# Performance work log

Hardware: AMD Instinct MI355X
Metric: run time of the kernel (lower is better)

The kernel has to match this reference:

```python
import jax, jax.numpy as jnp
import numpy as np

B, S, D = 2, 2048, 1024
H, HK, HD = 16, 4, 64          # query heads, kv heads, head dim = D//H
WIN = 1024                     # sliding attention window
E, K, DH = 8, 2, 2048          # experts, top_k, expert hidden (== d_head ctor arg)
ATTN_EPS, FFN_EPS = 1e-5, 1e-6
ROPE_THETA = 10000.0


def setup_inputs() -> dict:
    key = jax.random.key(0)
    ks = jax.random.split(key, 9)
    sc = 0.02
    # real rotary frequencies for positions [start_pos, start_pos+S)
    start_pos = 0
    inv_freq = 1.0 / (ROPE_THETA ** (jnp.arange(0, HD, 2, dtype=jnp.float32) / HD))  # [HD//2]
    pos = jnp.arange(start_pos, start_pos + S, dtype=jnp.float32)
    ang = pos[:, None] * inv_freq[None, :]  # [S, HD//2]
    return {
        'x': jax.random.normal(ks[0], (B, S, D), jnp.float32),
        'freqs_cos': jnp.cos(ang),
        'freqs_sin': jnp.sin(ang),
        'attn_norm_w': jnp.ones((D,), jnp.float32),
        'wq': jax.random.normal(ks[1], (D, H * HD), jnp.float32) * sc,
        'wk': jax.random.normal(ks[2], (D, HK * HD), jnp.float32) * sc,
        'wv': jax.random.normal(ks[3], (D, HK * HD), jnp.float32) * sc,
        'wo': jax.random.normal(ks[4], (H * HD, D), jnp.float32) * sc,
        'ffn_norm_w': jnp.ones((D,), jnp.float32),
        'router_w': jax.random.normal(ks[5], (D, E), jnp.float32) * sc,
        'w1': jax.random.normal(ks[6], (E, D, DH), jnp.float32) * sc,
        'w2': jax.random.normal(ks[7], (E, DH, D), jnp.float32) * sc,
        'start_pos': start_pos,
    }


def _rmsnorm(x, w, eps):
    return x * jax.lax.rsqrt(jnp.mean(x * x, axis=-1, keepdims=True) + eps) * w


def _rope(t, cos, sin):
    # t: [B,S,N,HD]; cos/sin: [S,HD//2] -> complex rotation on consecutive pairs
    shp = t.shape
    t = t.reshape(shp[:-1] + (HD // 2, 2))
    t0, t1 = t[..., 0], t[..., 1]
    c = cos[None, :, None, :]
    s = sin[None, :, None, :]
    r = jnp.stack([t0 * c - t1 * s, t0 * s + t1 * c], axis=-1)
    return r.reshape(shp)


def reference(x, freqs_cos, freqs_sin, attn_norm_w, wq, wk, wv, wo,
              ffn_norm_w, router_w, w1, w2, start_pos):
    # ---- attention sublayer (RMSNorm -> GQA sliding-window attn) ----
    hn = _rmsnorm(x, attn_norm_w, ATTN_EPS)
    q = (hn @ wq).reshape(B, S, H, HD)
    k = (hn @ wk).reshape(B, S, HK, HD)
    v = (hn @ wv).reshape(B, S, HK, HD)
    q = _rope(q, freqs_cos, freqs_sin)
    k = _rope(k, freqs_cos, freqs_sin)
    rep = H // HK
    k = jnp.repeat(k, rep, axis=2)  # [B,S,H,HD]
    v = jnp.repeat(v, rep, axis=2)
    scale = 1.0 / np.sqrt(HD).astype(np.float32)
    scores = jnp.einsum('bqhd,bkhd->bhqk', q, k) * scale  # [B,H,S,S]
    qi = jnp.arange(S) + start_pos
    kj = jnp.arange(S) + start_pos
    mask = (kj[None, :] <= qi[:, None]) & (qi[:, None] - kj[None, :] < WIN)
    scores = jnp.where(mask[None, None], scores, jnp.float32(-1e30))
    attn = jax.nn.softmax(scores, axis=-1)
    o = jnp.einsum('bhqk,bkhd->bqhd', attn, v).reshape(B, S, H * HD)
    h = x + o @ wo

    # ---- MoE sublayer (RMSNorm -> router top-k -> expert FFNs) ----
    fn = _rmsnorm(h, ffn_norm_w, FFN_EPS).reshape(-1, D)  # [T,D], T=B*S
    probs = jax.nn.softmax(fn @ router_w, axis=-1)        # [T,E]
    top_vals, top_idx = jax.lax.top_k(probs, K)           # [T,K]
    gates = top_vals / jnp.sum(top_vals, axis=-1, keepdims=True)
    gmat = jnp.sum(jax.nn.one_hot(top_idx, E, dtype=fn.dtype) * gates[..., None], axis=1)  # [T,E]
    moe = jnp.zeros_like(fn)
    for e in range(E):  # fixed small expert count
        moe = moe + gmat[:, e:e + 1] * (jax.nn.silu(fn @ w1[e]) @ w2[e])
    return h + moe.reshape(B, S, D)
```

## Files before the change

kernel.cpp:

```cpp
#include <hip/hip_runtime.h>
#include <hip/hip_bf16.h>

using bf16 = __hip_bfloat16;
typedef __attribute__((ext_vector_type(8))) short bf16x8;
typedef __attribute__((ext_vector_type(4))) short short4v;
typedef __attribute__((ext_vector_type(4))) float f32x4;

#define DEV static __device__ __forceinline__

DEV float b2f(bf16 v) { return __bfloat162float(v); }
DEV bf16  f2b(float f) { return __float2bfloat16(f); }
DEV short bbits(float f) { bf16 h = __float2bfloat16(f); short u; __builtin_memcpy(&u, &h, 2); return u; }
DEV float sb2f(short s) {
  unsigned u = ((unsigned)(unsigned short)s) << 16;
  float f; __builtin_memcpy(&f, &u, 4); return f;
}

#define GL2LDS(g, l)                                                        \
  __builtin_amdgcn_global_load_lds(                                         \
      (const __attribute__((address_space(1))) void*)(g),                   \
      (__attribute__((address_space(3))) void*)(l), 16, 0, 0)

__global__ __launch_bounds__(256) void transpose_convert(
    const float* __restrict__ src, bf16* __restrict__ dst, int K, int N) {
  __shared__ float tile[64][65];
  int n0 = blockIdx.x * 64, k0 = blockIdx.y * 64;
  size_t bo = (size_t)blockIdx.z * K * N;
  src += bo; dst += bo;
  int t = threadIdx.x;
  int rr = t >> 4, cc = (t & 15) * 4;
#pragma unroll
  for (int p = 0; p < 4; ++p) {
    int r = rr + p * 16;
    const float4 v = *(const float4*)&src[(size_t)(k0 + r) * N + n0 + cc];
    tile[r][cc] = v.x; tile[r][cc + 1] = v.y; tile[r][cc + 2] = v.z; tile[r][cc + 3] = v.w;
  }
  __syncthreads();
#pragma unroll
  for (int p = 0; p < 4; ++p) {
    int nr = rr + p * 16;
    short4v o;
    o[0] = bbits(tile[cc + 0][nr]);
    o[1] = bbits(tile[cc + 1][nr]);
    o[2] = bbits(tile[cc + 2][nr]);
    o[3] = bbits(tile[cc + 3][nr]);
    *(short4v*)&dst[(size_t)(n0 + nr) * K + k0 + cc] = o;
  }
}

__global__ __launch_bounds__(256) void rmsnorm_kernel(
    const float* __restrict__ x, const float* __restrict__ w,
    bf16* __restrict__ o, float eps) {
  int row = blockIdx.x;
  const float* xr = x + (size_t)row * 1024;
  int t = threadIdx.x;
  float4 v = *(const float4*)&xr[t * 4];
  float ss = v.x * v.x + v.y * v.y + v.z * v.z + v.w * v.w;
#pragma unroll
  for (int d = 32; d; d >>= 1) ss += __shfl_down(ss, d);
  __shared__ float red[4];
  if ((t & 63) == 0) red[t >> 6] = ss;
  __syncthreads();
  float sum = red[0] + red[1] + red[2] + red[3];
  float sc = rsqrtf(sum * (1.f / 1024.f) + eps);
  const float4 wv = *(const float4*)&w[t * 4];
  short4v pk;
  pk[0] = bbits(v.x * sc * wv.x);
  pk[1] = bbits(v.y * sc * wv.y);
  pk[2] = bbits(v.z * sc * wv.z);
  pk[3] = bbits(v.w * sc * wv.w);
  *(short4v*)&o[(size_t)row * 1024 + t * 4] = pk;
}

__global__ __launch_bounds__(256) void rope_kernel(
    bf16* __restrict__ tbuf, const float* __restrict__ fcos,
    const float* __restrict__ fsin, int ncols, int pshift) {
  int tid = blockIdx.x * 256 + threadIdx.x;
  int row = tid >> pshift;
  int cp = tid & ((1 << pshift) - 1);
  if (row >= 4096) return;
  int i = cp & 31;
  int s = row & 2047;
  bf16* p = tbuf + (size_t)row * ncols + cp * 2;
  float t0 = b2f(p[0]), t1 = b2f(p[1]);
  float c = fcos[s * 32 + i], sn = fsin[s * 32 + i];
  p[0] = f2b(t0 * c - t1 * sn);
  p[1] = f2b(t0 * sn + t1 * c);
}

template <int MODE>
__global__ __launch_bounds__(256) void gemm_bt(
    const bf16* __restrict__ A, const bf16* __restrict__ Bt,
    int M, int N, int Kd,
    bf16* __restrict__ outb, float* __restrict__ outf,
    const float* __restrict__ resid,
    const int* __restrict__ counts, const int* __restrict__ offsets,
    const int* __restrict__ tok, const float* __restrict__ gatel) {
  int count = M, off = 0;
  const bf16* Ap = A;
  const bf16* Bp = Bt;
  if (MODE == 2 || MODE == 3) {
    int e = blockIdx.z;
    count = counts[e]; off = offsets[e];
    Bp = Bt + (size_t)e * Kd * N;
    if (MODE == 3) Ap = A + (size_t)off * Kd;
  }
  int mb, nb;
  if (MODE == 2 || MODE == 3) {
    mb = blockIdx.y * 128; nb = blockIdx.x * 128;
  } else {
    int gx = gridDim.x;
    int flat = blockIdx.y * gx + blockIdx.x;
    int cpx = (gx * gridDim.y) >> 3;
    int swz = (flat & 7) * cpx + (flat >> 3);
    mb = (swz / gx) * 128; nb = (swz % gx) * 128;
  }
  if (mb >= count) return;

  __shared__ __align__(16) bf16 As[2][128 * 32];
  __shared__ __align__(16) bf16 Bs[2][128 * 32];

  int t = threadIdx.x;
  int lane = t & 63, wid = t >> 6;

  const bf16* agl[2];
  const bf16* bgl[2];
#pragma unroll
  for (int iss = 0; iss < 2; ++iss) {
    int p = iss * 256 + wid * 64 + lane;
    int row = p >> 2, cs = p & 3;
    int c = cs ^ (row & 3);
    int m = mb + row;
    const bf16* abase;
    if (MODE == 2) {
      int tokid = (m < count) ? tok[off + m] : 0;
      abase = A + (size_t)tokid * Kd;
    } else {
      int mm = (m < count) ? m : 0;
      abase = Ap + (size_t)mm * Kd;
    }
    agl[iss] = abase + c * 8;
    bgl[iss] = Bp + (size_t)(nb + row) * Kd + c * 8;
  }

  int wr = (wid >> 1) * 64, wc = (wid & 1) * 64;
  int lr = lane & 15, lkc = lane >> 4;

  auto stage = [&](int buf, int kt) {
#pragma unroll
    for (int iss = 0; iss < 2; ++iss) {
      GL2LDS(agl[iss] + kt * 32, &As[buf][(iss * 256 + wid * 64) * 8]);
      GL2LDS(bgl[iss] + kt * 32, &Bs[buf][(iss * 256 + wid * 64) * 8]);
    }
  };

  const f32x4 fzero = {0.f, 0.f, 0.f, 0.f};
  f32x4 acc[4][4];
#pragma unroll
  for (int i = 0; i < 4; ++i)
#pragma unroll
    for (int j = 0; j < 4; ++j) acc[i][j] = fzero;

  int nk = Kd >> 5;
  stage(0, 0);
  __syncthreads();
  for (int kt = 0; kt < nk; ++kt) {
    int cur = kt & 1;
    if (kt + 1 < nk) stage(cur ^ 1, kt + 1);
    bf16x8 af[4], bfr[4];
#pragma unroll
    for (int i = 0; i < 4; ++i) {
      int r = wr + i * 16 + lr;
      af[i] = *(const bf16x8*)&As[cur][r * 32 + ((lkc ^ (r & 3)) * 8)];
    }
#pragma unroll
    for (int j = 0; j < 4; ++j) {
      int r = wc + j * 16 + lr;
      bfr[j] = *(const bf16x8*)&Bs[cur][r * 32 + ((lkc ^ (r & 3)) * 8)];
    }
#pragma unroll
    for (int i = 0; i < 4; ++i)
#pragma unroll
      for (int j = 0; j < 4; ++j)
        acc[i][j] = __builtin_amdgcn_mfma_f32_16x16x32_bf16(af[i], bfr[j], acc[i][j], 0, 0, 0);
    __syncthreads();
  }

  int rq = lane >> 4;
#pragma unroll
  for (int i = 0; i < 4; ++i) {
#pragma unroll
    for (int j = 0; j < 4; ++j) {
      if (MODE == 4) {
        int n = nb + wc + j * 16 + lr;
        int kh = n >> 6, d = n & 63;
        int m0 = mb + wr + i * 16 + rq * 4;
        int bb = m0 >> 11, s = m0 & 2047;
        short4v pk;
#pragma unroll
        for (int r = 0; r < 4; ++r) pk[r] = bbits(acc[i][j][r]);
        *(short4v*)&outb[((size_t)((bb * 4 + kh) * 64 + d)) * 2048 + s] = pk;
      } else {
#pragma unroll
        for (int r = 0; r < 4; ++r) {
          int m = mb + wr + i * 16 + rq * 4 + r;
          int n = nb + wc + j * 16 + lr;
          float v = acc[i][j][r];
          if (MODE == 0) {
            outb[(size_t)m * N + n] = f2b(v);
          } else if (MODE == 1) {
            outf[(size_t)m * N + n] = resid[(size_t)m * N + n] + v;
          } else if (MODE == 2) {
            if (m < count) {
              float sg = 1.f / (1.f + expf(-v));
              outb[(size_t)(off + m) * N + n] = f2b(v * sg);
            }
          } else if (MODE == 3) {
            if (m < count) {
              int row = off + m;
              outb[(size_t)row * N + n] = f2b(gatel[row] * v);
            }
          }
        }
      }
    }
  }
}

__global__ __launch_bounds__(256) void attn_kernel(
    const bf16* __restrict__ q, const bf16* __restrict__ kb,
    const bf16* __restrict__ vt, bf16* __restrict__ o) {
  int qb = blockIdx.x, h = blockIdx.y, b = blockIdx.z;
  int kh = h >> 2;
  int t = threadIdx.x;
  int lane = t & 63, wid = t >> 6;
  int lr = lane & 15, lkc = lane >> 4;
  int q0 = qb * 64;
  int qrow = q0 + wid * 16;

  __shared__ __align__(16) bf16 Ks[64 * 64];
  __shared__ __align__(16) bf16 Vs[64 * 64];
  __shared__ __align__(16) bf16 Ps[4][16 * 72];

  bf16x8 aq[2];
#pragma unroll
  for (int kk = 0; kk < 2; ++kk)
    aq[kk] = *(const bf16x8*)&q[(size_t)(b * 2048 + qrow + lr) * 1024 + h * 64 + kk * 32 + lkc * 8];

  const f32x4 fzero = {0.f, 0.f, 0.f, 0.f};
  f32x4 oacc[4];
  float mrun[4], lrun[4];
#pragma unroll
  for (int r = 0; r < 4; ++r) { oacc[r] = fzero; mrun[r] = -1e30f; lrun[r] = 0.f; }

  int klo = q0 - 1023; if (klo < 0) klo = 0;
  int tlo = klo >> 6, thi = q0 >> 6;
  int skey = t >> 3;
  int sch = t & 7;

  for (int kt = tlo; kt <= thi; ++kt) {
    int kbase = kt * 64;
#pragma unroll
    for (int pp = 0; pp < 2; ++pp) {
      int key = skey + pp * 32;
      bf16x8 kv = *(const bf16x8*)&kb[(size_t)(b * 2048 + kbase + key) * 256 + kh * 64 + sch * 8];
      *(bf16x8*)&Ks[key * 64 + ((sch ^ (key & 7)) * 8)] = kv;
      bf16x8 vv = *(const bf16x8*)&vt[((size_t)((b * 4 + kh) * 64 + key)) * 2048 + kbase + sch * 8];
      *(bf16x8*)&Vs[key * 64 + ((sch ^ (key & 7)) * 8)] = vv;
    }
    __syncthreads();

    f32x4 sacc[4];
#pragma unroll
    for (int nt = 0; nt < 4; ++nt) sacc[nt] = fzero;
#pragma unroll
    for (int nt = 0; nt < 4; ++nt)
#pragma unroll
      for (int kk = 0; kk < 2; ++kk) {
        int r = nt * 16 + lr;
        bf16x8 bk = *(const bf16x8*)&Ks[r * 64 + (((kk * 4 + lkc) ^ (r & 7)) * 8)];
        sacc[nt] = __builtin_amdgcn_mfma_f32_16x16x32_bf16(aq[kk], bk, sacc[nt], 0, 0, 0);
      }

    float sval[4][4], mt[4];
    int qg = qrow + lkc * 4;
#pragma unroll
    for (int r = 0; r < 4; ++r) mt[r] = -1e30f;
#pragma unroll
    for (int nt = 0; nt < 4; ++nt) {
      int kkey = kbase + nt * 16 + lr;
#pragma unroll
      for (int r = 0; r < 4; ++r) {
        float s = sacc[nt][r] * 0.125f;
        int qq = qg + r;
        bool valid = (kkey <= qq) && (qq - kkey < 1024);
        s = valid ? s : -1e30f;
        sval[nt][r] = s;
        mt[r] = fmaxf(mt[r], s);
      }
    }
#pragma unroll
    for (int d = 1; d < 16; d <<= 1)
#pragma unroll
      for (int r = 0; r < 4; ++r) mt[r] = fmaxf(mt[r], __shfl_xor(mt[r], d));
    float alpha[4], rs[4];
#pragma unroll
    for (int r = 0; r < 4; ++r) {
      float mn = fmaxf(mrun[r], mt[r]);
      alpha[r] = __expf(mrun[r] - mn);
      mrun[r] = mn;
      rs[r] = 0.f;
    }
#pragma unroll
    for (int nt = 0; nt < 4; ++nt)
#pragma unroll
      for (int r = 0; r < 4; ++r) {
        float pv = __expf(sval[nt][r] - mrun[r]);
        sval[nt][r] = pv;
        rs[r] += pv;
      }
#pragma unroll
    for (int d = 1; d < 16; d <<= 1)
#pragma unroll
      for (int r = 0; r < 4; ++r) rs[r] += __shfl_xor(rs[r], d);
#pragma unroll
    for (int r = 0; r < 4; ++r) lrun[r] = lrun[r] * alpha[r] + rs[r];
#pragma unroll
    for (int dt = 0; dt < 4; ++dt) {
      f32x4 t4 = oacc[dt];
#pragma unroll
      for (int r = 0; r < 4; ++r) t4[r] *= alpha[r];
      oacc[dt] = t4;
    }

    bf16* pw = &Ps[wid][0];
#pragma unroll
    for (int nt = 0; nt < 4; ++nt)
#pragma unroll
      for (int r = 0; r < 4; ++r)
        pw[(lkc * 4 + r) * 72 + nt * 16 + lr] = f2b(sval[nt][r]);
    __syncthreads();

    bf16x8 pa[2];
#pragma unroll
    for (int kk2 = 0; kk2 < 2; ++kk2)
      pa[kk2] = *(const bf16x8*)&pw[lr * 72 + kk2 * 32 + lkc * 8];
#pragma unroll
    for (int dt = 0; dt < 4; ++dt)
#pragma unroll
      for (int kk2 = 0; kk2 < 2; ++kk2) {
        int rrow = dt * 16 + lr;
        bf16x8 bv = *(const bf16x8*)&Vs[rrow * 64 + (((kk2 * 4 + lkc) ^ (rrow & 7)) * 8)];
        oacc[dt] = __builtin_amdgcn_mfma_f32_16x16x32_bf16(pa[kk2], bv, oacc[dt], 0, 0, 0);
      }
    __syncthreads();
  }

#pragma unroll
  for (int dt = 0; dt < 4; ++dt)
#pragma unroll
    for (int r = 0; r < 4; ++r) {
      int qq = qrow + lkc * 4 + r;
      int dd = dt * 16 + lr;
      o[(size_t)(b * 2048 + qq) * 1024 + h * 64 + dd] = f2b(oacc[dt][r] / lrun[r]);
    }
}

__global__ __launch_bounds__(256) void router_kernel(
    const float* __restrict__ h, const float* __restrict__ ffnw,
    const float* __restrict__ rw, float* __restrict__ gates,
    int* __restrict__ eidx) {
  int wid = threadIdx.x >> 6, lane = threadIdx.x & 63;
  int row = blockIdx.x * 4 + wid;
  const float* hr = h + (size_t)row * 1024;
  float xs[16];
  float ss = 0.f;
#pragma unroll
  for (int i = 0; i < 16; ++i) { float f = hr[lane + i * 64]; xs[i] = f; ss += f * f; }
#pragma unroll
  for (int d = 32; d; d >>= 1) ss += __shfl_xor(ss, d);
  float sc = rsqrtf(ss * (1.f / 1024.f) + 1e-6f);
  float lg[8];
#pragma unroll
  for (int e = 0; e < 8; ++e) lg[e] = 0.f;
#pragma unroll
  for (int i = 0; i < 16; ++i) {
    int d = lane + i * 64;
    float f = xs[i] * sc * ffnw[d];
    const float* rr = rw + d * 8;
#pragma unroll
    for (int e = 0; e < 8; ++e) lg[e] += f * rr[e];
  }
#pragma unroll
  for (int d = 32; d; d >>= 1)
#pragma unroll
    for (int e = 0; e < 8; ++e) lg[e] += __shfl_xor(lg[e], d);
  if (lane == 0) {
    int e0 = 0; float v0 = lg[0];
#pragma unroll
    for (int e = 1; e < 8; ++e) if (lg[e] > v0) { v0 = lg[e]; e0 = e; }
    int e1 = -1; float v1 = -1e30f;
#pragma unroll
    for (int e = 0; e < 8; ++e) if (e != e0 && lg[e] > v1) { v1 = lg[e]; e1 = e; }
    float r1 = expf(v1 - v0);
    float den = 1.f + r1;
    gates[row * 2] = 1.f / den;
    gates[row * 2 + 1] = r1 / den;
    eidx[row * 2] = e0;
    eidx[row * 2 + 1] = e1;
  }
}

__global__ __launch_bounds__(1024) void moe_setup(
    const int* __restrict__ eidx, const float* __restrict__ gates,
    int* __restrict__ counts, int* __restrict__ offsets,
    int* __restrict__ tok, float* __restrict__ gatel, int* __restrict__ inv) {
  __shared__ int hist[8];
  __shared__ int cur[8];
  int t = threadIdx.x;
  if (t < 8) hist[t] = 0;
  __syncthreads();
  int e[8];
#pragma unroll
  for (int c = 0; c < 8; ++c) {
    e[c] = eidx[c * 1024 + t];
    atomicAdd(&hist[e[c]], 1);
  }
  __syncthreads();
  if (t == 0) {
    int o = 0;
#pragma unroll
    for (int i = 0; i < 8; ++i) {
      offsets[i] = o; cur[i] = o;
      int cnt = hist[i]; counts[i] = cnt; o += cnt;
    }
  }
  __syncthreads();
#pragma unroll
  for (int c = 0; c < 8; ++c) {
    int i = c * 1024 + t;
    int pos = atomicAdd(&cur[e[c]], 1);
    tok[pos] = i >> 1;
    gatel[pos] = gates[i];
    inv[i] = pos;
  }
}

__global__ __launch_bounds__(256) void final_add(
    const float* __restrict__ h, const bf16* __restrict__ y2,
    const int* __restrict__ inv, float* __restrict__ out) {
  int tokid = blockIdx.x;
  int t = threadIdx.x;
  int i0 = inv[tokid * 2], i1 = inv[tokid * 2 + 1];
  size_t base = (size_t)tokid * 1024 + t * 4;
  float4 a = *(const float4*)&h[base];
  short4v p0 = *(const short4v*)&y2[(size_t)i0 * 1024 + t * 4];
  short4v p1 = *(const short4v*)&y2[(size_t)i1 * 1024 + t * 4];
  float4 o;
  o.x = a.x + sb2f(p0[0]) + sb2f(p1[0]);
  o.y = a.y + sb2f(p0[1]) + sb2f(p1[1]);
  o.z = a.z + sb2f(p0[2]) + sb2f(p1[2]);
  o.w = a.w + sb2f(p0[3]) + sb2f(p1[3]);
  *(float4*)&out[base] = o;
}

extern "C" void kernel_launch(void* const* d_in, const int* in_sizes, int n_in,
                              void* d_out, int out_size, void* d_ws, size_t ws_size,
                              hipStream_t stream) {
  const float* x    = (const float*)d_in[0];
  const float* fcos = (const float*)d_in[1];
  const float* fsin = (const float*)d_in[2];
  const float* attw = (const float*)d_in[3];
  const float* wq   = (const float*)d_in[4];
  const float* wk   = (const float*)d_in[5];
  const float* wv   = (const float*)d_in[6];
  const float* wo   = (const float*)d_in[7];
  const float* ffnw = (const float*)d_in[8];
  const float* rw   = (const float*)d_in[9];
  const float* w1   = (const float*)d_in[10];
  const float* w2   = (const float*)d_in[11];
  float* out = (float*)d_out;

  const int M = 4096;
  char* p = (char*)d_ws;
  auto alloc = [&](size_t b) { char* r = p; p += (b + 255) & ~(size_t)255; return r; };

  bf16* hn    = (bf16*)alloc((size_t)M * 1024 * 2);
  bf16* qb    = (bf16*)alloc((size_t)M * 1024 * 2);
  bf16* kbuf  = (bf16*)alloc((size_t)M * 256 * 2);
  bf16* vt    = (bf16*)alloc((size_t)M * 256 * 2);
  bf16* ob    = (bf16*)alloc((size_t)M * 1024 * 2);
  float* hbuf = (float*)alloc((size_t)M * 1024 * 4);
  bf16* fn    = (bf16*)alloc((size_t)M * 1024 * 2);
  bf16* wqt   = (bf16*)alloc((size_t)1024 * 1024 * 2);
  bf16* wkt   = (bf16*)alloc((size_t)256 * 1024 * 2);
  bf16* wvt   = (bf16*)alloc((size_t)256 * 1024 * 2);
  bf16* wot   = (bf16*)alloc((size_t)1024 * 1024 * 2);
  bf16* w1t   = (bf16*)alloc((size_t)8 * 2048 * 1024 * 2);
  bf16* w2t   = (bf16*)alloc((size_t)8 * 1024 * 2048 * 2);
  bf16* act   = (bf16*)alloc((size_t)8192 * 2048 * 2);
  bf16* y2    = (bf16*)alloc((size_t)8192 * 1024 * 2);
  float* gates = (float*)alloc((size_t)M * 2 * 4);
  int* eidx    = (int*)alloc((size_t)M * 2 * 4);
  int* counts  = (int*)alloc(8 * 4);
  int* offsets = (int*)alloc(8 * 4);
  int* tok     = (int*)alloc(8192 * 4);
  int* inv     = (int*)alloc(8192 * 4);
  float* gatel = (float*)alloc(8192 * 4);

  transpose_convert<<<dim3(16, 16, 1), 256, 0, stream>>>(wq, wqt, 1024, 1024);
  transpose_convert<<<dim3(4, 16, 1), 256, 0, stream>>>(wk, wkt, 1024, 256);
  transpose_convert<<<dim3(4, 16, 1), 256, 0, stream>>>(wv, wvt, 1024, 256);
  transpose_convert<<<dim3(16, 16, 1), 256, 0, stream>>>(wo, wot, 1024, 1024);
  transpose_convert<<<dim3(32, 16, 8), 256, 0, stream>>>(w1, w1t, 1024, 2048);
  transpose_convert<<<dim3(16, 32, 8), 256, 0, stream>>>(w2, w2t, 2048, 1024);

  rmsnorm_kernel<<<M, 256, 0, stream>>>(x, attw, hn, 1e-5f);

  gemm_bt<0><<<dim3(8, 32, 1), 256, 0, stream>>>(hn, wqt, M, 1024, 1024, qb, nullptr, nullptr,
      nullptr, nullptr, nullptr, nullptr);
  gemm_bt<0><<<dim3(2, 32, 1), 256, 0, stream>>>(hn, wkt, M, 256, 1024, kbuf, nullptr, nullptr,
      nullptr, nullptr, nullptr, nullptr);
  gemm_bt<4><<<dim3(2, 32, 1), 256, 0, stream>>>(hn, wvt, M, 256, 1024, vt, nullptr, nullptr,
      nullptr, nullptr, nullptr, nullptr);

  rope_kernel<<<(M * 512) / 256, 256, 0, stream>>>(qb, fcos, fsin, 1024, 9);
  rope_kernel<<<(M * 128) / 256, 256, 0, stream>>>(kbuf, fcos, fsin, 256, 7);

  attn_kernel<<<dim3(32, 16, 2), 256, 0, stream>>>(qb, kbuf, vt, ob);

  gemm_bt<1><<<dim3(8, 32, 1), 256, 0, stream>>>(ob, wot, M, 1024, 1024, nullptr, hbuf, x,
      nullptr, nullptr, nullptr, nullptr);

  rmsnorm_kernel<<<M, 256, 0, stream>>>(hbuf, ffnw, fn, 1e-6f);

  router_kernel<<<M / 4, 256, 0, stream>>>(hbuf, ffnw, rw, gates, eidx);
  moe_setup<<<1, 1024, 0, stream>>>(eidx, gates, counts, offsets, tok, gatel, inv);

  gemm_bt<2><<<dim3(16, 64, 8), 256, 0, stream>>>(fn, w1t, M, 2048, 1024, act, nullptr, nullptr,
      counts, offsets, tok, nullptr);
  gemm_bt<3><<<dim3(8, 64, 8), 256, 0, stream>>>(act, w2t, M, 1024, 2048, y2, nullptr, nullptr,
      counts, offsets, tok, gatel);

  final_add<<<M, 256, 0, stream>>>(hbuf, y2, inv, out);
}
```

Baseline: 395.3 us.

## Fuse QKV projections, merge RoPE launches, fuse FFN rmsnorm with router

Q, K and V weights are packed into one transposed matrix, so a single GEMM writes Q and K row-major and V transposed. This replaces three GEMM launches and lets the normalized input be read once. The two RoPE launches become one kernel, and the FFN rmsnorm and router are merged into a block-per-row kernel that reuses the normalized values for the router logits. The MoE grids are also reordered so the expert index sits on the y dimension and the m-tile on z, which changes block scheduling order. The cost is per-element branching in the fused GEMM epilogue.

```diff
diff --git a/kernel.cpp b/kernel.cpp
--- a/kernel.cpp
+++ b/kernel.cpp
@@ -25,8 +25,8 @@
     const float* __restrict__ src, bf16* __restrict__ dst, int K, int N) {
   __shared__ float tile[64][65];
   int n0 = blockIdx.x * 64, k0 = blockIdx.y * 64;
-  size_t bo = (size_t)blockIdx.z * K * N;
-  src += bo; dst += bo;
+  src += (size_t)blockIdx.z * K * N;
+  dst += (size_t)blockIdx.z * K * N;
   int t = threadIdx.x;
   int rr = t >> 4, cc = (t & 15) * 4;
 #pragma unroll
@@ -72,18 +72,79 @@
   *(short4v*)&o[(size_t)row * 1024 + t * 4] = pk;
 }
 
-__global__ __launch_bounds__(256) void rope_kernel(
-    bf16* __restrict__ tbuf, const float* __restrict__ fcos,
-    const float* __restrict__ fsin, int ncols, int pshift) {
+__global__ __launch_bounds__(256) void rmsnorm_router(
+    const float* __restrict__ h, const float* __restrict__ w,
+    const float* __restrict__ rw, bf16* __restrict__ fn,
+    float* __restrict__ gates, int* __restrict__ eidx) {
+  int row = blockIdx.x;
+  const float* hr = h + (size_t)row * 1024;
+  int t = threadIdx.x;
+  float4 v = *(const float4*)&hr[t * 4];
+  float ss = v.x * v.x + v.y * v.y + v.z * v.z + v.w * v.w;
+#pragma unroll
+  for (int d = 32; d; d >>= 1) ss += __shfl_down(ss, d);
+  __shared__ float red[4];
+  __shared__ float red2[4][8];
+  if ((t & 63) == 0) red[t >> 6] = ss;
+  __syncthreads();
+  float sum = red[0] + red[1] + red[2] + red[3];
+  float sc = rsqrtf(sum * (1.f / 1024.f) + 1e-6f);
+  const float4 wv = *(const float4*)&w[t * 4];
+  float f0 = v.x * sc * wv.x, f1 = v.y * sc * wv.y;
+  float f2 = v.z * sc * wv.z, f3 = v.w * sc * wv.w;
+  short4v pk;
+  pk[0] = bbits(f0); pk[1] = bbits(f1); pk[2] = bbits(f2); pk[3] = bbits(f3);
+  *(short4v*)&fn[(size_t)row * 1024 + t * 4] = pk;
+  const float* rr = rw + (size_t)t * 4 * 8;
+  float lg[8];
+#pragma unroll
+  for (int e = 0; e < 8; ++e)
+    lg[e] = f0 * rr[e] + f1 * rr[8 + e] + f2 * rr[16 + e] + f3 * rr[24 + e];
+#pragma unroll
+  for (int d = 32; d; d >>= 1)
+#pragma unroll
+    for (int e = 0; e < 8; ++e) lg[e] += __shfl_down(lg[e], d);
+  if ((t & 63) == 0)
+#pragma unroll
+    for (int e = 0; e < 8; ++e) red2[t >> 6][e] = lg[e];
+  __syncthreads();
+  if (t == 0) {
+    float L[8];
+#pragma unroll
+    for (int e = 0; e < 8; ++e)
+      L[e] = red2[0][e] + red2[1][e] + red2[2][e] + red2[3][e];
+    int e0 = 0; float v0 = L[0];
+#pragma unroll
+    for (int e = 1; e < 8; ++e) if (L[e] > v0) { v0 = L[e]; e0 = e; }
+    int e1 = -1; float v1 = -1e30f;
+#pragma unroll
+    for (int e = 0; e < 8; ++e) if (e != e0 && L[e] > v1) { v1 = L[e]; e1 = e; }
+    float r1 = expf(v1 - v0);
+    float den = 1.f + r1;
+    gates[row * 2] = 1.f / den;
+    gates[row * 2 + 1] = r1 / den;
+    eidx[row * 2] = e0;
+    eidx[row * 2 + 1] = e1;
+  }
+}
+
+__global__ __launch_bounds__(256) void rope_all(
+    bf16* __restrict__ qb, bf16* __restrict__ kbuf,
+    const float* __restrict__ fcos, const float* __restrict__ fsin) {
   int tid = blockIdx.x * 256 + threadIdx.x;
-  int row = tid >> pshift;
-  int cp = tid & ((1 << pshift) - 1);
-  if (row >= 4096) return;
-  int i = cp & 31;
-  int s = row & 2047;
-  bf16* p = tbuf + (size_t)row * ncols + cp * 2;
+  bf16* p; int srow, i;
+  if (tid < 2097152) {
+    int row = tid >> 9, cp = tid & 511;
+    p = qb + (size_t)row * 1024 + cp * 2;
+    srow = row & 2047; i = cp & 31;
+  } else {
+    int t2 = tid - 2097152;
+    int row = t2 >> 7, cp = t2 & 127;
+    p = kbuf + (size_t)row * 256 + cp * 2;
+    srow = row & 2047; i = cp & 31;
+  }
   float t0 = b2f(p[0]), t1 = b2f(p[1]);
-  float c = fcos[s * 32 + i], sn = fsin[s * 32 + i];
+  float c = fcos[srow * 32 + i], sn = fsin[srow * 32 + i];
   p[0] = f2b(t0 * c - t1 * sn);
   p[1] = f2b(t0 * sn + t1 * c);
 }
@@ -92,22 +153,20 @@
 __global__ __launch_bounds__(256) void gemm_bt(
     const bf16* __restrict__ A, const bf16* __restrict__ Bt,
     int M, int N, int Kd,
-    bf16* __restrict__ outb, float* __restrict__ outf,
-    const float* __restrict__ resid,
+    bf16* __restrict__ outb, bf16* __restrict__ outk, bf16* __restrict__ outv,
+    float* __restrict__ outf, const float* __restrict__ resid,
     const int* __restrict__ counts, const int* __restrict__ offsets,
     const int* __restrict__ tok, const float* __restrict__ gatel) {
   int count = M, off = 0;
   const bf16* Ap = A;
   const bf16* Bp = Bt;
+  int mb, nb;
   if (MODE == 2 || MODE == 3) {
-    int e = blockIdx.z;
+    int e = blockIdx.y;
     count = counts[e]; off = offsets[e];
     Bp = Bt + (size_t)e * Kd * N;
     if (MODE == 3) Ap = A + (size_t)off * Kd;
-  }
-  int mb, nb;
-  if (MODE == 2 || MODE == 3) {
-    mb = blockIdx.y * 128; nb = blockIdx.x * 128;
+    mb = blockIdx.z * 128; nb = blockIdx.x * 128;
   } else {
     int gx = gridDim.x;
     int flat = blockIdx.y * gx + blockIdx.x;
@@ -191,24 +250,33 @@
   for (int i = 0; i < 4; ++i) {
 #pragma unroll
     for (int j = 0; j < 4; ++j) {
-      if (MODE == 4) {
+      if (MODE == 5) {
         int n = nb + wc + j * 16 + lr;
-        int kh = n >> 6, d = n & 63;
-        int m0 = mb + wr + i * 16 + rq * 4;
-        int bb = m0 >> 11, s = m0 & 2047;
-        short4v pk;
-#pragma unroll
-        for (int r = 0; r < 4; ++r) pk[r] = bbits(acc[i][j][r]);
-        *(short4v*)&outb[((size_t)((bb * 4 + kh) * 64 + d)) * 2048 + s] = pk;
+        if (n >= 1280) {
+          int vcol = n - 1280;
+          int kh = vcol >> 6, d = vcol & 63;
+          int m0 = mb + wr + i * 16 + rq * 4;
+          int bb = m0 >> 11, s = m0 & 2047;
+          short4v pk;
+#pragma unroll
+          for (int r = 0; r < 4; ++r) pk[r] = bbits(acc[i][j][r]);
+          *(short4v*)&outv[((size_t)((bb * 4 + kh) * 64 + d)) * 2048 + s] = pk;
+        } else {
+#pragma unroll
+          for (int r = 0; r < 4; ++r) {
+            int m = mb + wr + i * 16 + rq * 4 + r;
+            float v = acc[i][j][r];
+            if (n < 1024) outb[(size_t)m * 1024 + n] = f2b(v);
+            else          outk[(size_t)m * 256 + (n - 1024)] = f2b(v);
+          }
+        }
       } else {
 #pragma unroll
         for (int r = 0; r < 4; ++r) {
           int m = mb + wr + i * 16 + rq * 4 + r;
           int n = nb + wc + j * 16 + lr;
           float v = acc[i][j][r];
-          if (MODE == 0) {
-            outb[(size_t)m * N + n] = f2b(v);
-          } else if (MODE == 1) {
+          if (MODE == 1) {
             outf[(size_t)m * N + n] = resid[(size_t)m * N + n] + v;
           } else if (MODE == 2) {
             if (m < count) {
@@ -364,51 +432,6 @@
       int dd = dt * 16 + lr;
       o[(size_t)(b * 2048 + qq) * 1024 + h * 64 + dd] = f2b(oacc[dt][r] / lrun[r]);
     }
-}
-
-__global__ __launch_bounds__(256) void router_kernel(
-    const float* __restrict__ h, const float* __restrict__ ffnw,
-    const float* __restrict__ rw, float* __restrict__ gates,
-    int* __restrict__ eidx) {
-  int wid = threadIdx.x >> 6, lane = threadIdx.x & 63;
-  int row = blockIdx.x * 4 + wid;
-  const float* hr = h + (size_t)row * 1024;
-  float xs[16];
-  float ss = 0.f;
-#pragma unroll
-  for (int i = 0; i < 16; ++i) { float f = hr[lane + i * 64]; xs[i] = f; ss += f * f; }
-#pragma unroll
-  for (int d = 32; d; d >>= 1) ss += __shfl_xor(ss, d);
-  float sc = rsqrtf(ss * (1.f / 1024.f) + 1e-6f);
-  float lg[8];
-#pragma unroll
-  for (int e = 0; e < 8; ++e) lg[e] = 0.f;
-#pragma unroll
-  for (int i = 0; i < 16; ++i) {
-    int d = lane + i * 64;
-    float f = xs[i] * sc * ffnw[d];
-    const float* rr = rw + d * 8;
-#pragma unroll
-    for (int e = 0; e < 8; ++e) lg[e] += f * rr[e];
-  }
-#pragma unroll
-  for (int d = 32; d; d >>= 1)
-#pragma unroll
-    for (int e = 0; e < 8; ++e) lg[e] += __shfl_xor(lg[e], d);
-  if (lane == 0) {
-    int e0 = 0; float v0 = lg[0];
-#pragma unroll
-    for (int e = 1; e < 8; ++e) if (lg[e] > v0) { v0 = lg[e]; e0 = e; }
-    int e1 = -1; float v1 = -1e30f;
-#pragma unroll
-    for (int e = 0; e < 8; ++e) if (e != e0 && lg[e] > v1) { v1 = lg[e]; e1 = e; }
-    float r1 = expf(v1 - v0);
-    float den = 1.f + r1;
-    gates[row * 2] = 1.f / den;
-    gates[row * 2 + 1] = r1 / den;
-    eidx[row * 2] = e0;
-    eidx[row * 2 + 1] = e1;
-  }
 }
 
 __global__ __launch_bounds__(1024) void moe_setup(
@@ -485,21 +508,19 @@
   char* p = (char*)d_ws;
   auto alloc = [&](size_t b) { char* r = p; p += (b + 255) & ~(size_t)255; return r; };
 
-  bf16* hn    = (bf16*)alloc((size_t)M * 1024 * 2);
-  bf16* qb    = (bf16*)alloc((size_t)M * 1024 * 2);
-  bf16* kbuf  = (bf16*)alloc((size_t)M * 256 * 2);
-  bf16* vt    = (bf16*)alloc((size_t)M * 256 * 2);
-  bf16* ob    = (bf16*)alloc((size_t)M * 1024 * 2);
-  float* hbuf = (float*)alloc((size_t)M * 1024 * 4);
-  bf16* fn    = (bf16*)alloc((size_t)M * 1024 * 2);
-  bf16* wqt   = (bf16*)alloc((size_t)1024 * 1024 * 2);
-  bf16* wkt   = (bf16*)alloc((size_t)256 * 1024 * 2);
-  bf16* wvt   = (bf16*)alloc((size_t)256 * 1024 * 2);
-  bf16* wot   = (bf16*)alloc((size_t)1024 * 1024 * 2);
-  bf16* w1t   = (bf16*)alloc((size_t)8 * 2048 * 1024 * 2);
-  bf16* w2t   = (bf16*)alloc((size_t)8 * 1024 * 2048 * 2);
-  bf16* act   = (bf16*)alloc((size_t)8192 * 2048 * 2);
-  bf16* y2    = (bf16*)alloc((size_t)8192 * 1024 * 2);
+  bf16* hn     = (bf16*)alloc((size_t)M * 1024 * 2);
+  bf16* qb     = (bf16*)alloc((size_t)M * 1024 * 2);
+  bf16* kbuf   = (bf16*)alloc((size_t)M * 256 * 2);
+  bf16* vt     = (bf16*)alloc((size_t)M * 256 * 2);
+  bf16* ob     = (bf16*)alloc((size_t)M * 1024 * 2);
+  float* hbuf  = (float*)alloc((size_t)M * 1024 * 4);
+  bf16* fn     = (bf16*)alloc((size_t)M * 1024 * 2);
+  bf16* wqkvt  = (bf16*)alloc((size_t)1536 * 1024 * 2);
+  bf16* wot    = (bf16*)alloc((size_t)1024 * 1024 * 2);
+  bf16* w1t    = (bf16*)alloc((size_t)8 * 2048 * 1024 * 2);
+  bf16* w2t    = (bf16*)alloc((size_t)8 * 1024 * 2048 * 2);
+  bf16* act    = (bf16*)alloc((size_t)8192 * 2048 * 2);
+  bf16* y2     = (bf16*)alloc((size_t)8192 * 1024 * 2);
   float* gates = (float*)alloc((size_t)M * 2 * 4);
   int* eidx    = (int*)alloc((size_t)M * 2 * 4);
   int* counts  = (int*)alloc(8 * 4);
@@ -508,39 +529,32 @@
   int* inv     = (int*)alloc(8192 * 4);
   float* gatel = (float*)alloc(8192 * 4);
 
-  transpose_convert<<<dim3(16, 16, 1), 256, 0, stream>>>(wq, wqt, 1024, 1024);
-  transpose_convert<<<dim3(4, 16, 1), 256, 0, stream>>>(wk, wkt, 1024, 256);
-  transpose_convert<<<dim3(4, 16, 1), 256, 0, stream>>>(wv, wvt, 1024, 256);
+  transpose_convert<<<dim3(16, 16, 1), 256, 0, stream>>>(wq, wqkvt, 1024, 1024);
+  transpose_convert<<<dim3(4, 16, 1), 256, 0, stream>>>(wk, wqkvt + (size_t)1024 * 1024, 1024, 256);
+  transpose_convert<<<dim3(4, 16, 1), 256, 0, stream>>>(wv, wqkvt + (size_t)1280 * 1024, 1024, 256);
   transpose_convert<<<dim3(16, 16, 1), 256, 0, stream>>>(wo, wot, 1024, 1024);
   transpose_convert<<<dim3(32, 16, 8), 256, 0, stream>>>(w1, w1t, 1024, 2048);
   transpose_convert<<<dim3(16, 32, 8), 256, 0, stream>>>(w2, w2t, 2048, 1024);
 
   rmsnorm_kernel<<<M, 256, 0, stream>>>(x, attw, hn, 1e-5f);
 
-  gemm_bt<0><<<dim3(8, 32, 1), 256, 0, stream>>>(hn, wqt, M, 1024, 1024, qb, nullptr, nullptr,
-      nullptr, nullptr, nullptr, nullptr);
-  gemm_bt<0><<<dim3(2, 32, 1), 256, 0, stream>>>(hn, wkt, M, 256, 1024, kbuf, nullptr, nullptr,
-      nullptr, nullptr, nullptr, nullptr);
-  gemm_bt<4><<<dim3(2, 32, 1), 256, 0, stream>>>(hn, wvt, M, 256, 1024, vt, nullptr, nullptr,
-      nullptr, nullptr, nullptr, nullptr);
-
-  rope_kernel<<<(M * 512) / 256, 256, 0, stream>>>(qb, fcos, fsin, 1024, 9);
-  rope_kernel<<<(M * 128) / 256, 256, 0, stream>>>(kbuf, fcos, fsin, 256, 7);
+  gemm_bt<5><<<dim3(12, 32, 1), 256, 0, stream>>>(hn, wqkvt, M, 1536, 1024,
+      qb, kbuf, vt, nullptr, nullptr, nullptr, nullptr, nullptr, nullptr);
+
+  rope_all<<<10240, 256, 0, stream>>>(qb, kbuf, fcos, fsin);
 
   attn_kernel<<<dim3(32, 16, 2), 256, 0, stream>>>(qb, kbuf, vt, ob);
 
-  gemm_bt<1><<<dim3(8, 32, 1), 256, 0, stream>>>(ob, wot, M, 1024, 1024, nullptr, hbuf, x,
-      nullptr, nullptr, nullptr, nullptr);
-
-  rmsnorm_kernel<<<M, 256, 0, stream>>>(hbuf, ffnw, fn, 1e-6f);
-
-  router_kernel<<<M / 4, 256, 0, stream>>>(hbuf, ffnw, rw, gates, eidx);
+  gemm_bt<1><<<dim3(8, 32, 1), 256, 0, stream>>>(ob, wot, M, 1024, 1024,
+      nullptr, nullptr, nullptr, hbuf, x, nullptr, nullptr, nullptr, nullptr);
+
+  rmsnorm_router<<<M, 256, 0, stream>>>(hbuf, ffnw, rw, fn, gates, eidx);
   moe_setup<<<1, 1024, 0, stream>>>(eidx, gates, counts, offsets, tok, gatel, inv);
 
-  gemm_bt<2><<<dim3(16, 64, 8), 256, 0, stream>>>(fn, w1t, M, 2048, 1024, act, nullptr, nullptr,
-      counts, offsets, tok, nullptr);
-  gemm_bt<3><<<dim3(8, 64, 8), 256, 0, stream>>>(act, w2t, M, 1024, 2048, y2, nullptr, nullptr,
-      counts, offsets, tok, gatel);
+  gemm_bt<2><<<dim3(16, 8, 64), 256, 0, stream>>>(fn, w1t, M, 2048, 1024,
+      act, nullptr, nullptr, nullptr, nullptr, counts, offsets, tok, nullptr);
+  gemm_bt<3><<<dim3(8, 8, 64), 256, 0, stream>>>(act, w2t, M, 1024, 2048,
+      y2, nullptr, nullptr, nullptr, nullptr, counts, offsets, tok, gatel);
 
   final_add<<<M, 256, 0, stream>>>(hbuf, y2, inv, out);
 }
```

New measurement: 350.6 us. 1.13x faster.
